# Kernel tuning notes

Hardware: AMD Instinct MI355X
Metric: run time of the kernel (lower is better)

## Reference

```python
import jax, jax.numpy as jnp
import numpy as np
from jax import lax

# Model dims (match init_kwargs config)
HID = 2048      # hidden_size
NH = 64         # num_heads
P = 64          # head_dim
N = 128         # ssm_state_size
G = 1           # n_groups
CS = 256        # chunk_size
K = 4           # conv kernel
D_INNER = NH * P                  # 4096
CONV_DIM = D_INNER + 2 * G * N    # 4352
PROJ = D_INNER + CONV_DIM + NH    # 8512
EPS = 1e-5
BATCH, SEQ = 2, 2048


def setup_inputs() -> dict:
    key = jax.random.key(0)
    ks = jax.random.split(key, 8)
    hidden_states = jax.random.normal(ks[0], (BATCH, SEQ, HID), dtype=jnp.float32)
    W_in = jax.random.normal(ks[1], (PROJ, HID), dtype=jnp.float32) * 0.02
    conv_w = jax.random.normal(ks[2], (CONV_DIM, 1, K), dtype=jnp.float32) * 0.2
    conv_b = jax.random.normal(ks[3], (CONV_DIM,), dtype=jnp.float32) * 0.02
    # dt_bias initialized like inv-softplus of dt in [1e-3, 1e-1]
    dt = jnp.exp(jax.random.uniform(ks[4], (NH,)) * (np.log(0.1) - np.log(0.001)) + np.log(0.001))
    dt_bias = (dt + jnp.log(-jnp.expm1(-dt))).astype(jnp.float32)
    A_log = jnp.log(jnp.arange(1, NH + 1, dtype=jnp.float32))
    D_param = jnp.ones((NH,), dtype=jnp.float32)
    norm_w = jnp.ones((D_INNER,), dtype=jnp.float32)
    W_out = jax.random.normal(ks[5], (HID, D_INNER), dtype=jnp.float32) * 0.02
    return {"hidden_states": hidden_states, "W_in": W_in, "conv_w": conv_w,
            "conv_b": conv_b, "dt_bias": dt_bias, "A_log": A_log,
            "D_param": D_param, "norm_w": norm_w, "W_out": W_out}


def _segsum(x):
    # x: (..., c) -> (..., c, c); seg[i, j] = sum_{j < k <= i} x_k (diag 0), -inf above diag
    T = x.shape[-1]
    xc = jnp.cumsum(x, axis=-1)
    seg = xc[..., :, None] - xc[..., None, :]
    mask = jnp.tril(jnp.ones((T, T), dtype=bool))
    return jnp.where(mask, seg, -jnp.inf)


def _mamba2_forward(hidden_states, W_in, conv_w, conv_b, dt_bias, A_log, D_param, norm_w, W_out):
    B_, L_ = hidden_states.shape[:2]
    proj = hidden_states @ W_in.T                           # (b, l, PROJ)
    z = proj[..., :D_INNER]                                 # gate
    xBC = proj[..., D_INNER:D_INNER + CONV_DIM]
    dt = proj[..., D_INNER + CONV_DIM:]                     # (b, l, NH)

    # depthwise causal conv1d + silu
    xc = lax.conv_general_dilated(
        jnp.transpose(xBC, (0, 2, 1)), conv_w,
        window_strides=(1,), padding=[(K - 1, 0)],
        feature_group_count=CONV_DIM)                        # (b, CONV_DIM, l)
    xc = xc + conv_b[None, :, None]
    xBC = jax.nn.silu(jnp.transpose(xc, (0, 2, 1)))          # (b, l, CONV_DIM)

    x = xBC[..., :D_INNER].reshape(B_, L_, NH, P)
    Bm = xBC[..., D_INNER:D_INNER + G * N].reshape(B_, L_, G, N)
    Cm = xBC[..., D_INNER + G * N:].reshape(B_, L_, G, N)

    dt = jax.nn.softplus(dt + dt_bias)                       # (b, l, NH)
    A = -jnp.exp(A_log)                                      # (NH,)

    Bh = jnp.repeat(Bm, NH // G, axis=2)                     # (b, l, h, n)
    Ch = jnp.repeat(Cm, NH // G, axis=2)

    # ---- chunked SSD scan ----
    nc = L_ // CS
    x_dt = (x * dt[..., None]).reshape(B_, nc, CS, NH, P)    # (b, c, s, h, p)
    B_c = Bh.reshape(B_, nc, CS, NH, N)
    C_c = Ch.reshape(B_, nc, CS, NH, N)
    dA = jnp.transpose((dt * A).reshape(B_, nc, CS, NH), (0, 3, 1, 2))  # (b, h, c, s)
    A_cum = jnp.cumsum(dA, axis=-1)                          # (b, h, c, s)

    Lmat = jnp.exp(_segsum(dA))                              # (b, h, c, s, s)
    Y_diag = jnp.einsum('bclhn,bcshn,bhcls,bcshp->bclhp', C_c, B_c, Lmat, x_dt)

    decay_states = jnp.exp(A_cum[..., -1:] - A_cum)          # (b, h, c, s)
    states = jnp.einsum('bclhn,bhcl,bclhp->bchpn', B_c, decay_states, x_dt)

    da_last = A_cum[..., -1]                                 # (b, h, c)

    def step(prev, inp):
        s_k, d_k = inp                                       # (b,h,p,n), (b,h)
        new = prev * jnp.exp(d_k)[..., None, None] + s_k
        return new, prev

    _, prev_states = lax.scan(step, jnp.zeros((B_, NH, P, N), dtype=x.dtype),
                              (jnp.transpose(states, (1, 0, 2, 3, 4)),
                               jnp.transpose(da_last, (2, 0, 1))))
    prev_states = jnp.transpose(prev_states, (1, 2, 0, 3, 4))  # (b, h, c, p, n)

    Y_off = jnp.einsum('bclhn,bhcpn,bhcl->bclhp', C_c, prev_states, jnp.exp(A_cum))

    y = (Y_diag + Y_off).reshape(B_, L_, NH, P) + D_param[None, None, :, None] * x
    y = y.reshape(B_, L_, D_INNER)

    # gated grouped RMSNorm (norm_before_gate=False): norm(y * silu(z)) * w
    g = y * jax.nn.silu(z)
    gs = D_INNER // G
    gr = g.reshape(B_, L_, G, gs)
    var = jnp.mean(gr * gr, axis=-1, keepdims=True)
    gn = (gr * lax.rsqrt(var + EPS)).reshape(B_, L_, D_INNER) * norm_w

    return gn @ W_out.T                                      # (b, l, HID)


def reference(hidden_states, W_in, conv_w, conv_b, dt_bias, A_log, D_param, norm_w, W_out):
    return _mamba2_forward(hidden_states, W_in, conv_w, conv_b, dt_bias, A_log, D_param, norm_w, W_out)
```

## Files before the change

### kernel.cpp

```cpp
#include <hip/hip_runtime.h>

#define SEQLEN 2048
#define NHEADS 64
#define PDIM 64
#define NSTATE 128
#define CSIZE 256
#define NCHUNK 8
#define DINNER 4096
#define CONVD 4352
#define PROJD 8512

using s8v = __attribute__((ext_vector_type(8))) short;
using f4v = __attribute__((ext_vector_type(4))) float;
using bf8v = __attribute__((ext_vector_type(8))) __bf16;

__device__ __forceinline__ short f2bf(float x) {
  union { float f; unsigned u; } t; t.f = x;
  unsigned r = t.u + 0x7FFFu + ((t.u >> 16) & 1u);
  return (short)(r >> 16);
}
__device__ __forceinline__ float bf2f(short s) {
  union { unsigned u; float f; } t;
  t.u = ((unsigned)(unsigned short)s) << 16;
  return t.f;
}

__device__ __forceinline__ f4v mfma_bf16(s8v a, s8v b, f4v c) {
  return __builtin_amdgcn_mfma_f32_16x16x32_bf16(
      __builtin_bit_cast(bf8v, a), __builtin_bit_cast(bf8v, b), c, 0, 0, 0);
}

__device__ __forceinline__ void gll16(const void* g, void* l) {
  __builtin_amdgcn_global_load_lds(
      (const __attribute__((address_space(1))) unsigned*)g,
      (__attribute__((address_space(3))) unsigned*)l, 16, 0, 0);
}

__global__ __launch_bounds__(256) void cast_bf16_kernel(
    const float* __restrict__ in, short* __restrict__ out, int n4) {
  int i = blockIdx.x * 256 + threadIdx.x;
  if (i < n4) {
    float4 v = ((const float4*)in)[i];
    short4 o;
    o.x = f2bf(v.x); o.y = f2bf(v.y); o.z = f2bf(v.z); o.w = f2bf(v.w);
    ((short4*)out)[i] = o;
  }
}


#define G1_STAGE_A(dst, h, kt) do {                                          \
    _Pragma("unroll")                                                        \
    for (int it_ = 0; it_ < 2; ++it_) {                                      \
      int ci_ = it_ * 512 + tid;                                             \
      int r_ = ci_ >> 3;                                                     \
      int g_ = ((ci_ & 7) ^ (r_ & 7)) << 3;                                  \
      gll16(&A[(size_t)(tm0 + (h) * 128 + r_) * 2048 + (kt) * 64 + g_],      \
            &(dst)[(h) * 8192 + ci_ * 8]);                                   \
    }                                                                        \
  } while (0)

#define G1_STAGE_B(dst, h, kt) do {                                          \
    _Pragma("unroll")                                                        \
    for (int it_ = 0; it_ < 2; ++it_) {                                      \
      int ci_ = it_ * 512 + tid;                                             \
      int r_ = ci_ >> 3;                                                     \
      int g_ = ((ci_ & 7) ^ (r_ & 7)) << 3;                                  \
      int br_ = tn0 + (h) * 128 + r_;                                        \
      if (br_ > 8511) br_ = 8511;       \
      gll16(&B[(size_t)br_ * 2048 + (kt) * 64 + g_],                         \
            &(dst)[(h) * 8192 + ci_ * 8]);                                   \
    }                                                                        \
  } while (0)

#define RD_A(m, ks) \
  (*(const s8v*)&Ad[(wm + (m) * 16 + lr) * 64 + (((ks) * 4 + q) ^ sw7) * 8])
#define RD_B(n, ks) \
  (*(const s8v*)&Bd[(wn + (n) * 16 + lr) * 64 + (((ks) * 4 + q) ^ sw7) * 8])

#define G1_MFMA2(m0, x00, x01, x10, x11) do {                                \
    __builtin_amdgcn_s_setprio(1);                                           \
    _Pragma("unroll") for (int n = 0; n < 4; ++n)                            \
      acc[m0][n] = mfma_bf16(x00, bk0[n], acc[m0][n]);                       \
    _Pragma("unroll") for (int n = 0; n < 4; ++n)                            \
      acc[m0][n] = mfma_bf16(x01, bk1[n], acc[m0][n]);                       \
    _Pragma("unroll") for (int n = 0; n < 4; ++n)                            \
      acc[(m0) + 1][n] = mfma_bf16(x10, bk0[n], acc[(m0) + 1][n]);           \
    _Pragma("unroll") for (int n = 0; n < 4; ++n)                            \
      acc[(m0) + 1][n] = mfma_bf16(x11, bk1[n], acc[(m0) + 1][n]);           \
    __builtin_amdgcn_s_setprio(0);                                           \
  } while (0)

__global__ __launch_bounds__(512, 2) void gemm1_256(
    const short* __restrict__ A, const short* __restrict__ B,
    short* __restrict__ z, short* __restrict__ xbc, float* __restrict__ dtb) {
  const int NT = 32;
  const int bid = blockIdx.x;
  const int sid = (bid & 7) * 68 + (bid >> 3);
  const int panel = sid / 136, rem = sid % 136;
  const int bx = rem >> 2, by = panel * 4 + (rem & 3);
  const int tm0 = by * 256, tn0 = bx * 256;
  __shared__ alignas(16) short lds[65536];
  const int tid = threadIdx.x;
  const int lane = tid & 63, wid = tid >> 6;
  const int wm = (wid >> 2) * 128, wn = (wid & 3) * 64;
  const int lr = lane & 15, q = lane >> 4;
  const int sw7 = lr & 7;

  f4v acc[8][4];
#pragma unroll
  for (int m = 0; m < 8; ++m)
#pragma unroll
    for (int n = 0; n < 4; ++n)
#pragma unroll
      for (int r = 0; r < 4; ++r) acc[m][n][r] = 0.f;

  {
    short* A0 = lds;
    short* B0 = lds + 16384;
    short* B1 = lds + 49152;
    G1_STAGE_A(A0, 0, 0); G1_STAGE_A(A0, 1, 0);
    G1_STAGE_B(B0, 0, 0); G1_STAGE_B(B0, 1, 0);
    G1_STAGE_B(B1, 0, 1); G1_STAGE_B(B1, 1, 1);
    asm volatile("s_waitcnt vmcnt(4)" ::: "memory");
    __builtin_amdgcn_s_barrier();
  }

  for (int t = 0; t < NT; ++t) {
    short* Ad = lds + ((t & 1) << 15);
    short* Bd = Ad + 16384;
    short* An = lds + (((t + 1) & 1) << 15);
    s8v bk0[4], bk1[4];
    {
#pragma unroll
      for (int n = 0; n < 4; ++n) { bk0[n] = RD_B(n, 0); bk1[n] = RD_B(n, 1); }
      s8v a00 = RD_A(0, 0), a01 = RD_A(0, 1);
      s8v a10 = RD_A(1, 0), a11 = RD_A(1, 1);
      if (t + 1 < NT) G1_STAGE_A(An, 0, t + 1);
      __builtin_amdgcn_s_barrier();
      asm volatile("s_waitcnt lgkmcnt(0)" ::: "memory");
      G1_MFMA2(0, a00, a01, a10, a11);
      __builtin_amdgcn_s_barrier();
    }
    {
      s8v a00 = RD_A(2, 0), a01 = RD_A(2, 1);
      s8v a10 = RD_A(3, 0), a11 = RD_A(3, 1);
      if (t + 1 < NT) G1_STAGE_A(An, 1, t + 1);
      __builtin_amdgcn_s_barrier();
      asm volatile("s_waitcnt lgkmcnt(0)" ::: "memory");
      G1_MFMA2(2, a00, a01, a10, a11);
      __builtin_amdgcn_s_barrier();
    }
    {
      s8v a00 = RD_A(4, 0), a01 = RD_A(4, 1);
      s8v a10 = RD_A(5, 0), a11 = RD_A(5, 1);
      if (t + 2 < NT) G1_STAGE_B(Bd, 0, t + 2);
      __builtin_amdgcn_s_barrier();
      asm volatile("s_waitcnt lgkmcnt(0)" ::: "memory");
      G1_MFMA2(4, a00, a01, a10, a11);
      __builtin_amdgcn_s_barrier();
    }
    {
      s8v a00 = RD_A(6, 0), a01 = RD_A(6, 1);
      s8v a10 = RD_A(7, 0), a11 = RD_A(7, 1);
      if (t + 2 < NT) G1_STAGE_B(Bd, 1, t + 2);
      if (t < NT - 2) {
        asm volatile("s_waitcnt vmcnt(4)" ::: "memory");
      } else {
        asm volatile("s_waitcnt vmcnt(0)" ::: "memory");
      }
      __builtin_amdgcn_s_barrier();
      asm volatile("s_waitcnt lgkmcnt(0)" ::: "memory");
      G1_MFMA2(6, a00, a01, a10, a11);
      __builtin_amdgcn_s_barrier();
    }
  }

  if (bx == 33) {
    if (wn == 0) {
#pragma unroll
      for (int m = 0; m < 8; ++m)
#pragma unroll
        for (int n = 0; n < 4; ++n) {
          int col = n * 16 + lr;
#pragma unroll
          for (int r = 0; r < 4; ++r) {
            int row = tm0 + wm + m * 16 + q * 4 + r;
            dtb[(size_t)row * NHEADS + col] = acc[m][n][r];
          }
        }
    }
    return;
  }
  short* outp; int stride, colbase;
  if (bx < 16) { outp = z;   stride = DINNER; colbase = tn0; }
  else         { outp = xbc; stride = CONVD;  colbase = tn0 - DINNER; }
  short* Cs = lds;
  for (int h = 0; h < 2; ++h) {
    __syncthreads();
    if ((wid >> 2) == h) {
#pragma unroll
      for (int m = 0; m < 8; ++m)
#pragma unroll
        for (int n = 0; n < 4; ++n)
#pragma unroll
          for (int r = 0; r < 4; ++r)
            Cs[(m * 16 + q * 4 + r) * 264 + wn + n * 16 + lr] =
                f2bf(acc[m][n][r]);
    }
    __syncthreads();
#pragma unroll
    for (int itr = 0; itr < 8; ++itr) {
      int idx = itr * 512 + tid;
      int r = idx >> 5, c8 = (idx & 31) * 8;
      s8v v = *(const s8v*)&Cs[r * 264 + c8];
      *(s8v*)&outp[(size_t)(tm0 + h * 128 + r) * stride + colbase + c8] = v;
    }
  }
}

__global__ __launch_bounds__(256, 4) void gemm_nt_bf16(
    const short* __restrict__ A, const short* __restrict__ B,
    float* __restrict__ C, int M, int N, int K) {
  const int nbx = N >> 7;
  const int bid0 = blockIdx.x;
  const int bid = (bid0 & 7) * (gridDim.x >> 3) + (bid0 >> 3);
  const int panel = bid / (nbx * 4), rem = bid % (nbx * 4);
  const int bx = rem >> 2, by = panel * 4 + (rem & 3);
  const int tn0 = bx * 128, tm0 = by * 128;
  __shared__ alignas(16) short As[128 * 32];
  __shared__ alignas(16) short Bs[128 * 32];
  const int tid = threadIdx.x;
  const int lane = tid & 63, wid = tid >> 6;
  const int wm = (wid >> 1) * 64, wn = (wid & 1) * 64;
  const int lr = lane & 15, q = lane >> 4;
  const int fA = (lr & 3) ^ ((lr >> 2) & 3);
  const int qs = (q ^ fA) * 8;
  f4v acc[4][4];
  for (int i = 0; i < 4; i++)
    for (int j = 0; j < 4; j++)
      for (int r = 0; r < 4; r++) acc[i][j][r] = 0.f;

  for (int k0 = 0; k0 < K; k0 += 32) {
    __syncthreads();
    for (int it = 0; it < 2; it++) {
      int ci = it * 256 + tid;
      int row = ci >> 2;
      int cg = ((ci & 3) ^ (row & 3) ^ ((row >> 2) & 3)) << 3;
      gll16(&A[(size_t)(tm0 + row) * K + k0 + cg], &As[ci * 8]);
      gll16(&B[(size_t)(tn0 + row) * K + k0 + cg], &Bs[ci * 8]);
    }
    __syncthreads();
    s8v af[4], bfr[4];
    for (int i = 0; i < 4; i++) af[i]  = *(const s8v*)&As[(wm + i * 16 + lr) * 32 + qs];
    for (int j = 0; j < 4; j++) bfr[j] = *(const s8v*)&Bs[(wn + j * 16 + lr) * 32 + qs];
    for (int i = 0; i < 4; i++)
      for (int j = 0; j < 4; j++)
        acc[i][j] = mfma_bf16(af[i], bfr[j], acc[i][j]);
  }
  for (int i = 0; i < 4; i++)
    for (int j = 0; j < 4; j++) {
      int r0 = tm0 + wm + i * 16 + q * 4;
      int c0 = tn0 + wn + j * 16 + lr;
      for (int r = 0; r < 4; r++)
        C[(size_t)(r0 + r) * N + c0] = acc[i][j][r];
    }
}

__global__ __launch_bounds__(256) void conv_silu_kernel(
    const short* __restrict__ xbc, const float* __restrict__ conv_w,
    const float* __restrict__ conv_b, short* __restrict__ xBCc) {
  int cc = blockIdx.x * 256 + threadIdx.x;
  int bl = blockIdx.y;
  int b = bl >> 11, l = bl & 2047;
  float4 wv = *(const float4*)&conv_w[cc * 4];
  float wk[4] = {wv.x, wv.y, wv.z, wv.w};
  float acc = conv_b[cc];
  const short* pbase = xbc + (size_t)(b * SEQLEN) * CONVD + cc;
#pragma unroll
  for (int k = 0; k < 4; k++) {
    int ls = l - 3 + k;
    if (ls >= 0) acc += bf2f(pbase[(size_t)ls * CONVD]) * wk[k];
  }
  float sv = acc / (1.f + expf(-acc));
  xBCc[(size_t)bl * CONVD + cc] = f2bf(sv);
}

__global__ __launch_bounds__(256) void dt_kernel(
    float* __restrict__ dtb, const float* __restrict__ dt_bias) {
  int idx = blockIdx.x * 256 + threadIdx.x;
  int hh = idx & 63;
  float v = dtb[idx] + dt_bias[hh];
  dtb[idx] = (v > 20.f) ? v : log1pf(expf(v));
}

__global__ __launch_bounds__(256) void ssd_states_kernel(
    const short* __restrict__ xBCc, const float* __restrict__ dtp,
    const float* __restrict__ A_log, short* __restrict__ states,
    float* __restrict__ da_last) {
  const int blk = blockIdx.x;
  const int h = blk & 63, cc = (blk >> 6) & 7, b = blk >> 9;
  const int tid = threadIdx.x;
  __shared__ float dt_s[CSIZE], Acum[CSIZE], w_s[CSIZE];
  __shared__ float xw[64][64];
  __shared__ float Bt[64][NSTATE];
  const size_t row0 = (size_t)(b * SEQLEN + cc * CSIZE);
  dt_s[tid] = dtp[(row0 + tid) * NHEADS + h];
  __syncthreads();
  if (tid == 0) {
    float Aval = -expf(A_log[h]);
    float s = 0.f;
    for (int i = 0; i < CSIZE; i++) { s += dt_s[i]; Acum[i] = s * Aval; }
    da_last[(size_t)(b * NHEADS + h) * NCHUNK + cc] = Acum[CSIZE - 1];
  }
  __syncthreads();
  float total = Acum[CSIZE - 1];
  w_s[tid] = dt_s[tid] * expf(total - Acum[tid]);
  float acc[4][8];
  for (int a = 0; a < 4; a++) for (int j = 0; j < 8; j++) acc[a][j] = 0.f;
  const int pi = (tid & 15) * 4, ni = (tid >> 4) * 8;
  for (int lt = 0; lt < 4; lt++) {
    __syncthreads();
    for (int i = 0; i < 4; i++) {
      int idx = tid + i * 256;
      int r = idx >> 4, c4 = (idx & 15) << 2;
      short4 v = *(const short4*)&xBCc[(row0 + lt * 64 + r) * CONVD + h * PDIM + c4];
      float wl = w_s[lt * 64 + r];
      xw[r][c4 + 0] = bf2f(v.x) * wl;
      xw[r][c4 + 1] = bf2f(v.y) * wl;
      xw[r][c4 + 2] = bf2f(v.z) * wl;
      xw[r][c4 + 3] = bf2f(v.w) * wl;
    }
    for (int i = 0; i < 8; i++) {
      int idx = tid + i * 256;
      int r = idx >> 5, c4 = (idx & 31) << 2;
      short4 v = *(const short4*)&xBCc[(row0 + lt * 64 + r) * CONVD + DINNER + c4];
      Bt[r][c4 + 0] = bf2f(v.x);
      Bt[r][c4 + 1] = bf2f(v.y);
      Bt[r][c4 + 2] = bf2f(v.z);
      Bt[r][c4 + 3] = bf2f(v.w);
    }
    __syncthreads();
    for (int l = 0; l < 64; l++) {
      float4 xv = *(const float4*)&xw[l][pi];
      float4 b0 = *(const float4*)&Bt[l][ni];
      float4 b1 = *(const float4*)&Bt[l][ni + 4];
      float xa[4] = {xv.x, xv.y, xv.z, xv.w};
      float bb[8] = {b0.x, b0.y, b0.z, b0.w, b1.x, b1.y, b1.z, b1.w};
      for (int a = 0; a < 4; a++)
        for (int j = 0; j < 8; j++)
          acc[a][j] += xa[a] * bb[j];
    }
  }
  const size_t sbase = (((size_t)b * NCHUNK + cc) * NHEADS + h) * (PDIM * NSTATE);
  for (int a = 0; a < 4; a++) {
    short o[8];
    for (int j = 0; j < 8; j++) o[j] = f2bf(acc[a][j]);
    *(s8v*)&states[sbase + (size_t)(pi + a) * NSTATE + ni] = *(const s8v*)o;
  }
}

__global__ __launch_bounds__(256) void scan_kernel(
    short* __restrict__ states, const float* __restrict__ da_last) {
  const int bh = blockIdx.x >> 2, sl = blockIdx.x & 3;
  const int b = bh >> 6, h = bh & 63;
  const int tid = threadIdx.x;
  float prev[8];
  for (int i = 0; i < 8; i++) prev[i] = 0.f;
  for (int c = 0; c < NCHUNK; c++) {
    const size_t base = (((size_t)b * NCHUNK + c) * NHEADS + h) * (PDIM * NSTATE)
                      + sl * 2048;
    const float d = expf(da_last[(size_t)bh * NCHUNK + c]);
    for (int i = 0; i < 8; i++) {
      size_t e = base + tid + i * 256;
      float s = bf2f(states[e]);
      states[e] = f2bf(prev[i]);
      prev[i] = prev[i] * d + s;
    }
  }
}

__global__ __launch_bounds__(256) void ssd_y_kernel(
    const short* __restrict__ xBCc, const float* __restrict__ dtp,
    const float* __restrict__ A_log, const float* __restrict__ D_param,
    const short* __restrict__ prevs, short* __restrict__ y) {
  const int blk = blockIdx.x;
  const int h = blk & 63, cc = (blk >> 6) & 7, b = blk >> 9;
  const int tid = threadIdx.x;
  const int lane = tid & 63, w = tid >> 6;
  const int lr = lane & 15, q = lane >> 4;
  __shared__ float dt_s[CSIZE];
  __shared__ float Acum[CSIZE];
  __shared__ short C_s[64][136];
  __shared__ short BP_s[64][136];
  __shared__ short xdtT[64][72];
  __shared__ short Mt[64][72];
  const size_t row0 = (size_t)(b * SEQLEN + cc * CSIZE);
  dt_s[tid] = dtp[(row0 + tid) * NHEADS + h];
  __syncthreads();
  if (tid == 0) {
    float Aval = -expf(A_log[h]);
    float s = 0.f;
    for (int i = 0; i < CSIZE; i++) { s += dt_s[i]; Acum[i] = s * Aval; }
  }
  const float Dh = D_param[h];
  const size_t prevbase = (((size_t)b * NCHUNK + cc) * NHEADS + h) * (PDIM * NSTATE);
  const int wl0 = w * 16;

  for (int lt = 0; lt < 4; lt++) {
    __syncthreads();
    for (int i = 0; i < 4; i++) {
      int idx = tid + i * 256;
      int r = idx >> 4, c8 = (idx & 15) << 3;
      *(s8v*)&C_s[r][c8] =
          *(const s8v*)&xBCc[(row0 + lt * 64 + r) * CONVD + DINNER + NSTATE + c8];
      *(s8v*)&BP_s[r][c8] = *(const s8v*)&prevs[prevbase + (size_t)r * NSTATE + c8];
    }
    __syncthreads();
    f4v acc[4];
    for (int j = 0; j < 4; j++) for (int r = 0; r < 4; r++) acc[j][r] = 0.f;
    for (int ks = 0; ks < 4; ks++) {
      s8v a = *(const s8v*)&C_s[wl0 + lr][ks * 32 + q * 8];
      for (int j = 0; j < 4; j++) {
        s8v bb = *(const s8v*)&BP_s[j * 16 + lr][ks * 32 + q * 8];
        acc[j] = mfma_bf16(a, bb, acc[j]);
      }
    }
    for (int r = 0; r < 4; r++) {
      float e = __expf(Acum[lt * 64 + wl0 + q * 4 + r]);
      for (int j = 0; j < 4; j++) acc[j][r] *= e;
    }
    for (int st = 0; st <= lt; st++) {
      __syncthreads();
      for (int i = 0; i < 4; i++) {
        int idx = tid + i * 256;
        int r = idx >> 4, c8 = (idx & 15) << 3;
        *(s8v*)&BP_s[r][c8] =
            *(const s8v*)&xBCc[(row0 + st * 64 + r) * CONVD + DINNER + c8];
      }
      for (int i = 0; i < 4; i++) {
        int idx = tid + i * 256;
        int r = idx >> 4, c4 = (idx & 15) << 2;
        float dtv = dt_s[st * 64 + r];
        short4 v = *(const short4*)&xBCc[(row0 + st * 64 + r) * CONVD + h * PDIM + c4];
        xdtT[c4 + 0][r] = f2bf(bf2f(v.x) * dtv);
        xdtT[c4 + 1][r] = f2bf(bf2f(v.y) * dtv);
        xdtT[c4 + 2][r] = f2bf(bf2f(v.z) * dtv);
        xdtT[c4 + 3][r] = f2bf(bf2f(v.w) * dtv);
      }
      __syncthreads();
      f4v sacc[4];
      for (int j = 0; j < 4; j++) for (int r = 0; r < 4; r++) sacc[j][r] = 0.f;
      for (int ks = 0; ks < 4; ks++) {
        s8v a = *(const s8v*)&C_s[wl0 + lr][ks * 32 + q * 8];
        for (int j = 0; j < 4; j++) {
          s8v bb = *(const s8v*)&BP_s[j * 16 + lr][ks * 32 + q * 8];
          sacc[j] = mfma_bf16(a, bb, sacc[j]);
        }
      }
      int lbase = lt * 64 + wl0 + q * 4;
      for (int j = 0; j < 4; j++) {
        int sg = st * 64 + j * 16 + lr;
        for (int r = 0; r < 4; r++) {
          int ll = lbase + r;
          float m = (sg <= ll) ? sacc[j][r] * __expf(Acum[ll] - Acum[sg]) : 0.f;
          Mt[wl0 + q * 4 + r][j * 16 + lr] = f2bf(m);
        }
      }
      __syncthreads();
      for (int ss2 = 0; ss2 < 2; ss2++) {
        s8v a = *(const s8v*)&Mt[wl0 + lr][ss2 * 32 + q * 8];
        for (int j = 0; j < 4; j++) {
          s8v bb = *(const s8v*)&xdtT[j * 16 + lr][ss2 * 32 + q * 8];
          acc[j] = mfma_bf16(a, bb, acc[j]);
        }
      }
    }
    for (int j = 0; j < 4; j++)
      for (int r = 0; r < 4; r++) {
        int lrow = wl0 + q * 4 + r;
        int ll = lt * 64 + lrow;
        int p = j * 16 + lr;
        float xv = bf2f(xBCc[(row0 + ll) * CONVD + h * PDIM + p]);
        Mt[lrow][p] = f2bf(acc[j][r] + Dh * xv);
      }
    __syncthreads();
    for (int ps = 0; ps < 2; ps++) {
      int r = ps * 32 + (tid >> 3);
      int c8 = (tid & 7) * 8;
      s8v v = *(const s8v*)&Mt[r][c8];
      *(s8v*)&y[(row0 + lt * 64 + r) * DINNER + h * PDIM + c8] = v;
    }
  }
}

__global__ __launch_bounds__(256) void norm_kernel(
    const short* __restrict__ y, const short* __restrict__ z,
    const float* __restrict__ norm_w, short* __restrict__ g) {
  int bl = blockIdx.x, tid = threadIdx.x;
  const short4* yrow = (const short4*)(y + (size_t)bl * DINNER);
  const short4* zrow = (const short4*)(z + (size_t)bl * DINNER);
  float gv[16];
  float ss = 0.f;
  for (int i = 0; i < 4; i++) {
    short4 yv = yrow[tid + i * 256];
    short4 zv = zrow[tid + i * 256];
    float zf[4] = {bf2f(zv.x), bf2f(zv.y), bf2f(zv.z), bf2f(zv.w)};
    float yf[4] = {bf2f(yv.x), bf2f(yv.y), bf2f(yv.z), bf2f(yv.w)};
    for (int t = 0; t < 4; t++) {
      float gg = yf[t] * (zf[t] / (1.f + expf(-zf[t])));
      gv[i * 4 + t] = gg;
      ss += gg * gg;
    }
  }
  for (int off = 32; off > 0; off >>= 1) ss += __shfl_down(ss, off);
  __shared__ float red[4];
  __shared__ float rsS;
  if ((tid & 63) == 0) red[tid >> 6] = ss;
  __syncthreads();
  if (tid == 0) rsS = rsqrtf((red[0] + red[1] + red[2] + red[3]) * (1.f / 4096.f) + 1e-5f);
  __syncthreads();
  float rs = rsS;
  for (int i = 0; i < 4; i++) {
    int j4 = (tid + i * 256) * 4;
    float4 nw = *(const float4*)&norm_w[j4];
    short4 o;
    o.x = f2bf(gv[i * 4 + 0] * rs * nw.x);
    o.y = f2bf(gv[i * 4 + 1] * rs * nw.y);
    o.z = f2bf(gv[i * 4 + 2] * rs * nw.z);
    o.w = f2bf(gv[i * 4 + 3] * rs * nw.w);
    *(short4*)&g[(size_t)bl * DINNER + j4] = o;
  }
}

extern "C" void kernel_launch(void* const* d_in, const int* in_sizes, int n_in,
                              void* d_out, int out_size, void* d_ws, size_t ws_size,
                              hipStream_t stream) {
  const float* hidden  = (const float*)d_in[0];
  const float* W_in    = (const float*)d_in[1];
  const float* conv_w  = (const float*)d_in[2];
  const float* conv_b  = (const float*)d_in[3];
  const float* dt_bias = (const float*)d_in[4];
  const float* A_log   = (const float*)d_in[5];
  const float* D_param = (const float*)d_in[6];
  const float* norm_w  = (const float*)d_in[7];
  const float* W_out   = (const float*)d_in[8];
  float* out = (float*)d_out;

  char* ws = (char*)d_ws;
  short* z_bf  = (short*)(ws + 0);
  float* dtb   = (float*)(ws + 33554432);
  float* da_l  = (float*)(ws + 34603008);
  short* xbc_pre = (short*)(ws + 34607104);
  short* y_bf    = (short*)(ws + 34607104);
  short* hid_bf  = (short*)(ws + 70258688);
  short* win_bf  = (short*)(ws + 87035904);
  short* xBCc    = (short*)(ws + 70258688);
  short* states  = (short*)(ws + 105910272);
  short* g_bf    = (short*)(ws + 70258688);
  short* wout_bf = (short*)(ws + 105910272);
  if (ws_size < (size_t)122687488) return;

  cast_bf16_kernel<<<8192, 256, 0, stream>>>(hidden, hid_bf, 2097152);
  cast_bf16_kernel<<<17024, 256, 0, stream>>>(W_in, win_bf, 4358144);

  gemm1_256<<<544, 512, 0, stream>>>(hid_bf, win_bf, z_bf, xbc_pre, dtb);

  conv_silu_kernel<<<dim3(17, 4096), 256, 0, stream>>>(xbc_pre, conv_w, conv_b, xBCc);
  dt_kernel<<<1024, 256, 0, stream>>>(dtb, dt_bias);

  ssd_states_kernel<<<1024, 256, 0, stream>>>(xBCc, dtb, A_log, states, da_l);
  scan_kernel<<<512, 256, 0, stream>>>(states, da_l);
  ssd_y_kernel<<<1024, 256, 0, stream>>>(xBCc, dtb, A_log, D_param, states, y_bf);

  norm_kernel<<<4096, 256, 0, stream>>>(y_bf, z_bf, norm_w, g_bf);
  cast_bf16_kernel<<<8192, 256, 0, stream>>>(W_out, wout_bf, 2097152);

  gemm_nt_bf16<<<512, 256, 0, stream>>>(g_bf, wout_bf, out, 4096, 2048, 4096);
}
```

Baseline: 673.5 us.

## Retile output GEMM, fuse dt softplus into GEMM1, merge weight cast into norm

Replaces the simple 128x128 output GEMM with a 256x128-tile, 512-thread kernel. It uses a 64-wide K step, double-buffered swizzled LDS staging and interleaved prefetch, modelled on the input-projection GEMM. The dt bias-add and softplus are folded into the first GEMM's epilogue, which removes the separate dt kernel. The W_out bf16 cast is merged into the norm kernel's grid to cut one launch. sched_barrier hints are added to keep the staging loads ahead of the barriers. The output GEMM now launches only 256 blocks, which may underfill the GPU.

```diff
diff --git a/kernel.cpp b/kernel.cpp
--- a/kernel.cpp
+++ b/kernel.cpp
@@ -92,7 +92,8 @@
 
 __global__ __launch_bounds__(512, 2) void gemm1_256(
     const short* __restrict__ A, const short* __restrict__ B,
-    short* __restrict__ z, short* __restrict__ xbc, float* __restrict__ dtb) {
+    short* __restrict__ z, short* __restrict__ xbc, float* __restrict__ dtb,
+    const float* __restrict__ dt_bias) {
   const int NT = 32;
   const int bid = blockIdx.x;
   const int sid = (bid & 7) * 68 + (bid >> 3);
@@ -136,6 +137,7 @@
       s8v a00 = RD_A(0, 0), a01 = RD_A(0, 1);
       s8v a10 = RD_A(1, 0), a11 = RD_A(1, 1);
       if (t + 1 < NT) G1_STAGE_A(An, 0, t + 1);
+      __builtin_amdgcn_sched_barrier(0);
       __builtin_amdgcn_s_barrier();
       asm volatile("s_waitcnt lgkmcnt(0)" ::: "memory");
       G1_MFMA2(0, a00, a01, a10, a11);
@@ -145,6 +147,7 @@
       s8v a00 = RD_A(2, 0), a01 = RD_A(2, 1);
       s8v a10 = RD_A(3, 0), a11 = RD_A(3, 1);
       if (t + 1 < NT) G1_STAGE_A(An, 1, t + 1);
+      __builtin_amdgcn_sched_barrier(0);
       __builtin_amdgcn_s_barrier();
       asm volatile("s_waitcnt lgkmcnt(0)" ::: "memory");
       G1_MFMA2(2, a00, a01, a10, a11);
@@ -154,6 +157,7 @@
       s8v a00 = RD_A(4, 0), a01 = RD_A(4, 1);
       s8v a10 = RD_A(5, 0), a11 = RD_A(5, 1);
       if (t + 2 < NT) G1_STAGE_B(Bd, 0, t + 2);
+      __builtin_amdgcn_sched_barrier(0);
       __builtin_amdgcn_s_barrier();
       asm volatile("s_waitcnt lgkmcnt(0)" ::: "memory");
       G1_MFMA2(4, a00, a01, a10, a11);
@@ -163,6 +167,7 @@
       s8v a00 = RD_A(6, 0), a01 = RD_A(6, 1);
       s8v a10 = RD_A(7, 0), a11 = RD_A(7, 1);
       if (t + 2 < NT) G1_STAGE_B(Bd, 1, t + 2);
+      __builtin_amdgcn_sched_barrier(0);
       if (t < NT - 2) {
         asm volatile("s_waitcnt vmcnt(4)" ::: "memory");
       } else {
@@ -182,10 +187,13 @@
 #pragma unroll
         for (int n = 0; n < 4; ++n) {
           int col = n * 16 + lr;
+          float bias = dt_bias[col];
 #pragma unroll
           for (int r = 0; r < 4; ++r) {
             int row = tm0 + wm + m * 16 + q * 4 + r;
-            dtb[(size_t)row * NHEADS + col] = acc[m][n][r];
+            float v = acc[m][n][r] + bias;
+            float sp = (v > 20.f) ? v : log1pf(expf(v));
+            dtb[(size_t)row * NHEADS + col] = sp;
           }
         }
     }
@@ -218,51 +226,142 @@
   }
 }
 
-__global__ __launch_bounds__(256, 4) void gemm_nt_bf16(
-    const short* __restrict__ A, const short* __restrict__ B,
-    float* __restrict__ C, int M, int N, int K) {
-  const int nbx = N >> 7;
-  const int bid0 = blockIdx.x;
-  const int bid = (bid0 & 7) * (gridDim.x >> 3) + (bid0 >> 3);
-  const int panel = bid / (nbx * 4), rem = bid % (nbx * 4);
+
+#define G2_STAGE_A(dst, h, kt) do {                                          \
+    _Pragma("unroll")                                                        \
+    for (int it_ = 0; it_ < 2; ++it_) {                                      \
+      int ci_ = it_ * 512 + tid;                                             \
+      int r_ = ci_ >> 3;                                                     \
+      int g_ = ((ci_ & 7) ^ (r_ & 7)) << 3;                                  \
+      gll16(&Ag[(size_t)(tm0 + (h) * 128 + r_) * 4096 + (kt) * 64 + g_],     \
+            &(dst)[(h) * 8192 + ci_ * 8]);                                   \
+    }                                                                        \
+  } while (0)
+
+#define G2_STAGE_B(dst, h, kt) do {                                          \
+    int ci_ = tid;                                                           \
+    int r_ = ci_ >> 3;                                                       \
+    int g_ = ((ci_ & 7) ^ (r_ & 7)) << 3;                                    \
+    gll16(&Bg[(size_t)(tn0 + (h) * 64 + r_) * 4096 + (kt) * 64 + g_],        \
+          &(dst)[(h) * 4096 + ci_ * 8]);                                     \
+  } while (0)
+
+#define RD_A2(m, ks) \
+  (*(const s8v*)&Ad[(wm + (m) * 16 + lr) * 64 + (((ks) * 4 + q) ^ sw7) * 8])
+#define RD_B2(n, ks) \
+  (*(const s8v*)&Bd[(wn + (n) * 16 + lr) * 64 + (((ks) * 4 + q) ^ sw7) * 8])
+
+#define G2_MFMA2(m0, x00, x01, x10, x11) do {                                \
+    __builtin_amdgcn_s_setprio(1);                                           \
+    _Pragma("unroll") for (int n = 0; n < 2; ++n)                            \
+      acc[m0][n] = mfma_bf16(x00, bk0[n], acc[m0][n]);                       \
+    _Pragma("unroll") for (int n = 0; n < 2; ++n)                            \
+      acc[m0][n] = mfma_bf16(x01, bk1[n], acc[m0][n]);                       \
+    _Pragma("unroll") for (int n = 0; n < 2; ++n)                            \
+      acc[(m0) + 1][n] = mfma_bf16(x10, bk0[n], acc[(m0) + 1][n]);           \
+    _Pragma("unroll") for (int n = 0; n < 2; ++n)                            \
+      acc[(m0) + 1][n] = mfma_bf16(x11, bk1[n], acc[(m0) + 1][n]);           \
+    __builtin_amdgcn_s_setprio(0);                                           \
+  } while (0)
+
+__global__ __launch_bounds__(512, 2) void gemm2_256x128(
+    const short* __restrict__ Ag, const short* __restrict__ Bg,
+    float* __restrict__ C) {
+  const int NT = 64;
+  const int bid = blockIdx.x;
+  const int sid = (bid & 7) * 32 + (bid >> 3);
+  const int panel = sid >> 6, rem = sid & 63;
   const int bx = rem >> 2, by = panel * 4 + (rem & 3);
-  const int tn0 = bx * 128, tm0 = by * 128;
-  __shared__ alignas(16) short As[128 * 32];
-  __shared__ alignas(16) short Bs[128 * 32];
+  const int tm0 = by * 256, tn0 = bx * 128;
+  __shared__ alignas(16) short lds[49152];
   const int tid = threadIdx.x;
   const int lane = tid & 63, wid = tid >> 6;
-  const int wm = (wid >> 1) * 64, wn = (wid & 1) * 64;
+  const int wm = (wid >> 2) * 128, wn = (wid & 3) * 32;
   const int lr = lane & 15, q = lane >> 4;
-  const int fA = (lr & 3) ^ ((lr >> 2) & 3);
-  const int qs = (q ^ fA) * 8;
-  f4v acc[4][4];
-  for (int i = 0; i < 4; i++)
-    for (int j = 0; j < 4; j++)
-      for (int r = 0; r < 4; r++) acc[i][j][r] = 0.f;
-
-  for (int k0 = 0; k0 < K; k0 += 32) {
-    __syncthreads();
-    for (int it = 0; it < 2; it++) {
-      int ci = it * 256 + tid;
-      int row = ci >> 2;
-      int cg = ((ci & 3) ^ (row & 3) ^ ((row >> 2) & 3)) << 3;
-      gll16(&A[(size_t)(tm0 + row) * K + k0 + cg], &As[ci * 8]);
-      gll16(&B[(size_t)(tn0 + row) * K + k0 + cg], &Bs[ci * 8]);
-    }
-    __syncthreads();
-    s8v af[4], bfr[4];
-    for (int i = 0; i < 4; i++) af[i]  = *(const s8v*)&As[(wm + i * 16 + lr) * 32 + qs];
-    for (int j = 0; j < 4; j++) bfr[j] = *(const s8v*)&Bs[(wn + j * 16 + lr) * 32 + qs];
-    for (int i = 0; i < 4; i++)
-      for (int j = 0; j < 4; j++)
-        acc[i][j] = mfma_bf16(af[i], bfr[j], acc[i][j]);
-  }
-  for (int i = 0; i < 4; i++)
-    for (int j = 0; j < 4; j++) {
-      int r0 = tm0 + wm + i * 16 + q * 4;
-      int c0 = tn0 + wn + j * 16 + lr;
-      for (int r = 0; r < 4; r++)
-        C[(size_t)(r0 + r) * N + c0] = acc[i][j][r];
+  const int sw7 = lr & 7;
+
+  f4v acc[8][2];
+#pragma unroll
+  for (int m = 0; m < 8; ++m)
+#pragma unroll
+    for (int n = 0; n < 2; ++n)
+#pragma unroll
+      for (int r = 0; r < 4; ++r) acc[m][n][r] = 0.f;
+
+  {
+    short* A0 = lds;
+    short* B0 = lds + 16384;
+    short* B1 = lds + 40960;
+    G2_STAGE_A(A0, 0, 0); G2_STAGE_A(A0, 1, 0);
+    G2_STAGE_B(B0, 0, 0); G2_STAGE_B(B0, 1, 0);
+    G2_STAGE_B(B1, 0, 1); G2_STAGE_B(B1, 1, 1);
+    asm volatile("s_waitcnt vmcnt(2)" ::: "memory");
+    __builtin_amdgcn_s_barrier();
+  }
+
+  for (int t = 0; t < NT; ++t) {
+    short* Ad = lds + (t & 1) * 24576;
+    short* Bd = Ad + 16384;
+    short* An = lds + ((t + 1) & 1) * 24576;
+    s8v bk0[2], bk1[2];
+    {
+#pragma unroll
+      for (int n = 0; n < 2; ++n) { bk0[n] = RD_B2(n, 0); bk1[n] = RD_B2(n, 1); }
+      s8v a00 = RD_A2(0, 0), a01 = RD_A2(0, 1);
+      s8v a10 = RD_A2(1, 0), a11 = RD_A2(1, 1);
+      if (t + 1 < NT) G2_STAGE_A(An, 0, t + 1);
+      __builtin_amdgcn_sched_barrier(0);
+      __builtin_amdgcn_s_barrier();
+      asm volatile("s_waitcnt lgkmcnt(0)" ::: "memory");
+      G2_MFMA2(0, a00, a01, a10, a11);
+      __builtin_amdgcn_s_barrier();
+    }
+    {
+      s8v a00 = RD_A2(2, 0), a01 = RD_A2(2, 1);
+      s8v a10 = RD_A2(3, 0), a11 = RD_A2(3, 1);
+      if (t + 1 < NT) G2_STAGE_A(An, 1, t + 1);
+      __builtin_amdgcn_sched_barrier(0);
+      __builtin_amdgcn_s_barrier();
+      asm volatile("s_waitcnt lgkmcnt(0)" ::: "memory");
+      G2_MFMA2(2, a00, a01, a10, a11);
+      __builtin_amdgcn_s_barrier();
+    }
+    {
+      s8v a00 = RD_A2(4, 0), a01 = RD_A2(4, 1);
+      s8v a10 = RD_A2(5, 0), a11 = RD_A2(5, 1);
+      if (t + 2 < NT) G2_STAGE_B(Bd, 0, t + 2);
+      __builtin_amdgcn_sched_barrier(0);
+      __builtin_amdgcn_s_barrier();
+      asm volatile("s_waitcnt lgkmcnt(0)" ::: "memory");
+      G2_MFMA2(4, a00, a01, a10, a11);
+      __builtin_amdgcn_s_barrier();
+    }
+    {
+      s8v a00 = RD_A2(6, 0), a01 = RD_A2(6, 1);
+      s8v a10 = RD_A2(7, 0), a11 = RD_A2(7, 1);
+      if (t + 2 < NT) G2_STAGE_B(Bd, 1, t + 2);
+      __builtin_amdgcn_sched_barrier(0);
+      if (t < NT - 2) {
+        asm volatile("s_waitcnt vmcnt(2)" ::: "memory");
+      } else {
+        asm volatile("s_waitcnt vmcnt(0)" ::: "memory");
+      }
+      __builtin_amdgcn_s_barrier();
+      asm volatile("s_waitcnt lgkmcnt(0)" ::: "memory");
+      G2_MFMA2(6, a00, a01, a10, a11);
+      __builtin_amdgcn_s_barrier();
+    }
+  }
+
+#pragma unroll
+  for (int m = 0; m < 8; ++m)
+#pragma unroll
+    for (int n = 0; n < 2; ++n) {
+      int r0 = tm0 + wm + m * 16 + q * 4;
+      int c0 = tn0 + wn + n * 16 + lr;
+#pragma unroll
+      for (int r = 0; r < 4; ++r)
+        C[(size_t)(r0 + r) * 2048 + c0] = acc[m][n][r];
     }
 }
 
@@ -283,14 +382,6 @@
   }
   float sv = acc / (1.f + expf(-acc));
   xBCc[(size_t)bl * CONVD + cc] = f2bf(sv);
-}
-
-__global__ __launch_bounds__(256) void dt_kernel(
-    float* __restrict__ dtb, const float* __restrict__ dt_bias) {
-  int idx = blockIdx.x * 256 + threadIdx.x;
-  int hh = idx & 63;
-  float v = dtb[idx] + dt_bias[hh];
-  dtb[idx] = (v > 20.f) ? v : log1pf(expf(v));
 }
 
 __global__ __launch_bounds__(256) void ssd_states_kernel(
@@ -493,10 +584,23 @@
   }
 }
 
-__global__ __launch_bounds__(256) void norm_kernel(
+__global__ __launch_bounds__(256) void norm_cast_kernel(
     const short* __restrict__ y, const short* __restrict__ z,
-    const float* __restrict__ norm_w, short* __restrict__ g) {
+    const float* __restrict__ norm_w, short* __restrict__ g,
+    const float* __restrict__ wsrc, short* __restrict__ wdst) {
   int bl = blockIdx.x, tid = threadIdx.x;
+  if (bl >= 4096) {
+    int base = (bl - 4096) * 1024 + tid;
+#pragma unroll
+    for (int i = 0; i < 4; i++) {
+      int idx = base + i * 256;
+      float4 v = ((const float4*)wsrc)[idx];
+      short4 o;
+      o.x = f2bf(v.x); o.y = f2bf(v.y); o.z = f2bf(v.z); o.w = f2bf(v.w);
+      ((short4*)wdst)[idx] = o;
+    }
+    return;
+  }
   const short4* yrow = (const short4*)(y + (size_t)bl * DINNER);
   const short4* zrow = (const short4*)(z + (size_t)bl * DINNER);
   float gv[16];
@@ -563,17 +667,15 @@
   cast_bf16_kernel<<<8192, 256, 0, stream>>>(hidden, hid_bf, 2097152);
   cast_bf16_kernel<<<17024, 256, 0, stream>>>(W_in, win_bf, 4358144);
 
-  gemm1_256<<<544, 512, 0, stream>>>(hid_bf, win_bf, z_bf, xbc_pre, dtb);
+  gemm1_256<<<544, 512, 0, stream>>>(hid_bf, win_bf, z_bf, xbc_pre, dtb, dt_bias);
 
   conv_silu_kernel<<<dim3(17, 4096), 256, 0, stream>>>(xbc_pre, conv_w, conv_b, xBCc);
-  dt_kernel<<<1024, 256, 0, stream>>>(dtb, dt_bias);
 
   ssd_states_kernel<<<1024, 256, 0, stream>>>(xBCc, dtb, A_log, states, da_l);
   scan_kernel<<<512, 256, 0, stream>>>(states, da_l);
   ssd_y_kernel<<<1024, 256, 0, stream>>>(xBCc, dtb, A_log, D_param, states, y_bf);
 
-  norm_kernel<<<4096, 256, 0, stream>>>(y_bf, z_bf, norm_w, g_bf);
-  cast_bf16_kernel<<<8192, 256, 0, stream>>>(W_out, wout_bf, 2097152);
-
-  gemm_nt_bf16<<<512, 256, 0, stream>>>(g_bf, wout_bf, out, 4096, 2048, 4096);
-}
+  norm_cast_kernel<<<6144, 256, 0, stream>>>(y_bf, z_bf, norm_w, g_bf, W_out, wout_bf);
+
+  gemm2_256x128<<<256, 512, 0, stream>>>(g_bf, wout_bf, out);
+}
```

Result: slower. 692.8 us (+2.9%).
